# Kernel tuning notes

Measured on AMD Instinct MI355X. Metric: run time of the kernel, lower is better.

Reference implementation:

```python
import jax, jax.numpy as jnp
import numpy as np

B, D, N, C = 2048, 128, 100000, 100
T = 2.0


def setup_inputs() -> dict:
    key = jax.random.key(0)
    k1, k2, k3 = jax.random.split(key, 3)
    x = jax.random.normal(k1, (B, D), dtype=jnp.float32)
    Address = jax.random.normal(k2, (N, D), dtype=jnp.float32)
    M = jax.random.uniform(k3, (N, C), dtype=jnp.float32)
    return {"x": x, "Address": Address, "M": M}


def reference(x, Address, M):
    # dist[b,n] = ||x_b - A_n||_2 via the expanded quadratic form (same as torch mm+norms)
    sq = (-2.0 * (x @ Address.T)
          + jnp.sum(Address * Address, axis=1)[None, :]
          + jnp.sum(x * x, axis=1)[:, None])
    dist = jnp.sqrt(jnp.maximum(sq, 0.0))  # clamp guards fp roundoff negatives
    # softmin over addresses == softmax(-dist/T)
    soft_w = jax.nn.softmax(-dist / T, axis=1)  # (B, N)
    logits = soft_w @ M  # (B, n_classes)
    return logits
```

## Files before the change

### kernel.cpp

```cpp
#include <hip/hip_runtime.h>

#define NTOT 100000
#define BD 128
#define NC 100
#define CP 112
#define BROWS 2048
#define LOG2E 1.4426950408889634f

typedef short short8 __attribute__((ext_vector_type(8)));
typedef float f32x4 __attribute__((ext_vector_type(4)));

__device__ __forceinline__ unsigned short f2bf(float f) {
    union { float f; unsigned u; } v; v.f = f;
    unsigned r = v.u + 0x7FFFu + ((v.u >> 16) & 1u);
    return (unsigned short)(r >> 16);
}

__device__ __forceinline__ unsigned pkbf(float a, float b) {
    unsigned r;
    asm("v_cvt_pk_bf16_f32 %0, %1, %2" : "=v"(r) : "v"(a), "v"(b));
    return r;
}

__device__ __forceinline__ float rawsqrt(float x) {
    float r;
    asm("v_sqrt_f32 %0, %1" : "=v"(r) : "v"(x));
    return r;
}

__device__ __forceinline__ float rawexp2(float x) {
    float r;
    asm("v_exp_f32 %0, %1" : "=v"(r) : "v"(x));
    return r;
}

__device__ __forceinline__ void gload16(const void* g, void* l) {
    __builtin_amdgcn_global_load_lds((const __attribute__((address_space(1))) void*)g,
                                     (__attribute__((address_space(3))) void*)l, 16, 0, 0);
}

__global__ __launch_bounds__(256) void prep_A(const float* __restrict__ A,
                                              unsigned short* __restrict__ Abf,
                                              float* __restrict__ anorm) {
    const int tid = threadIdx.x;
    const int row = blockIdx.x * 16 + (tid >> 4);
    const int g = tid & 15;
    const float* src = A + (size_t)row * BD + g * 8;
    float4 v0 = *(const float4*)src, v1 = *(const float4*)(src + 4);
    uint4 u;
    u.x = pkbf(v0.x, v0.y); u.y = pkbf(v0.z, v0.w);
    u.z = pkbf(v1.x, v1.y); u.w = pkbf(v1.z, v1.w);
    float ss = v0.x*v0.x + v0.y*v0.y + v0.z*v0.z + v0.w*v0.w
             + v1.x*v1.x + v1.y*v1.y + v1.z*v1.z + v1.w*v1.w;
    ss += __shfl_xor(ss, 1); ss += __shfl_xor(ss, 2);
    ss += __shfl_xor(ss, 4); ss += __shfl_xor(ss, 8);
    *(uint4*)((char*)Abf + (size_t)row * 256 + ((g * 16) ^ ((row & 15) << 4))) = u;
    if (g == 0) anorm[row] = ss;
}

__global__ __launch_bounds__(256) void prep_M(const float* __restrict__ M,
                                              unsigned short* __restrict__ Mt) {
    __shared__ __align__(16) unsigned short lm[100 * 264];
    const int t = threadIdx.x;
    const int n0 = blockIdx.x * 256;
    const int rows = min(256, NTOT - n0);
    const float4* Mf4 = (const float4*)(M + (size_t)n0 * NC);
    #pragma unroll
    for (int k = 0; k < 25; ++k) {
        int f = k * 256 + t;
        if (f < rows * 25) {
            int row = (int)(((unsigned)f * 5243u) >> 17);
            int c4 = f - row * 25;
            float4 v = Mf4[f];
            lm[(c4 * 4 + 0) * 264 + row] = f2bf(v.x);
            lm[(c4 * 4 + 1) * 264 + row] = f2bf(v.y);
            lm[(c4 * 4 + 2) * 264 + row] = f2bf(v.z);
            lm[(c4 * 4 + 3) * 264 + row] = f2bf(v.w);
        }
    }
    __syncthreads();
    uint4* Mt4 = (uint4*)Mt;
    const int nb = rows >> 3;
    #pragma unroll
    for (int k = 0; k < 14; ++k) {
        int f = k * 256 + t;
        int c = f >> 5, nblk = f & 31;
        if (nblk < nb) {
            uint4 v = {0u, 0u, 0u, 0u};
            if (c < NC) v = *(const uint4*)&lm[c * 264 + nblk * 8];
            Mt4[(size_t)c * (NTOT / 8) + (n0 >> 3) + nblk] = v;
        }
    }
}

__global__ __launch_bounds__(256, 2) void fused_main(
    const float* __restrict__ x, const unsigned short* __restrict__ Abf,
    const float* __restrict__ anorm, const unsigned short* __restrict__ Mt,
    float* __restrict__ pO, float* __restrict__ pL,
    int cmask, int cshift, int qq, int rr)
{
    __shared__ __align__(16) unsigned short a_lds[2][4096];
    __shared__ __align__(16) unsigned short m_lds[2][3584];
    __shared__ __align__(16) unsigned short p_lds[8][640];

    const int tid = threadIdx.x, wave = tid >> 6, lane = tid & 63;
    const int l15 = lane & 15, lhi = lane >> 4;
    const int bid = blockIdx.x;
    const int chunk = bid & cmask, rg = bid >> cshift;
    const int ts = chunk * qq + (chunk < rr ? chunk : rr);
    const int tiles = (chunk < rr) ? qq + 1 : qq;
    const int n0c = ts * 32;
    const int qbw = rg * 128 + wave * 32;

    short8 qf[2][4];
    float nx[2];
    #pragma unroll
    for (int t = 0; t < 2; ++t) {
        float s = 0.f;
        #pragma unroll
        for (int kk = 0; kk < 4; ++kk) {
            const float* xp = x + (size_t)(qbw + t * 16 + l15) * BD + kk * 32 + lhi * 8;
            float4 v0 = *(const float4*)xp, v1 = *(const float4*)(xp + 4);
            uint4 uu;
            uu.x = pkbf(v0.x, v0.y); uu.y = pkbf(v0.z, v0.w);
            uu.z = pkbf(v1.x, v1.y); uu.w = pkbf(v1.z, v1.w);
            qf[t][kk] = *(short8*)&uu;
            s += v0.x*v0.x + v0.y*v0.y + v0.z*v0.z + v0.w*v0.w
               + v1.x*v1.x + v1.y*v1.y + v1.z*v1.z + v1.w*v1.w;
        }
        s += __shfl_xor(s, 16); s += __shfl_xor(s, 32);
        nx[t] = s;
    }

    const char* aFix = (const char*)Abf + tid * 16;
    const int r0 = tid >> 2, sg0 = ((tid & 3) - r0 - (r0 >> 2)) & 3;
    const char* mFix0 = (const char*)Mt + (size_t)r0 * (NTOT * 2) + sg0 * 16;
    const int L1 = tid + 256, r1 = L1 >> 2, sg1 = ((L1 & 3) - r1 - (r1 >> 2)) & 3;
    const char* mFix1 = (const char*)Mt + (size_t)r1 * (NTOT * 2) + sg1 * 16;

    auto stage = [&](int buf, int t) {
        const int n0 = n0c + t * 32;
        const char* ab = aFix + (size_t)n0 * 256;
        char* al = (char*)&a_lds[buf][0] + tid * 16;
        gload16(ab, al);
        gload16(ab + 4096, al + 4096);
        gload16(mFix0 + (size_t)n0 * 2, (char*)&m_lds[buf][0] + tid * 16);
        if (tid < 192)
            gload16(mFix1 + (size_t)n0 * 2, (char*)&m_lds[buf][0] + (tid + 256) * 16);
    };

    f32x4 Oacc[2][7];
    const f32x4 zf = {0.f, 0.f, 0.f, 0.f};
    #pragma unroll
    for (int t = 0; t < 2; ++t)
        #pragma unroll
        for (int c0 = 0; c0 < 7; ++c0) Oacc[t][c0] = zf;
    float lsum[2] = {0.f, 0.f};

    stage(0, 0);
    __syncthreads();

    for (int it = 0; it < tiles; ++it) {
        const int buf = it & 1;
        const int n0 = n0c + it * 32;
        if (it + 1 < tiles) stage(buf ^ 1, it + 1);

        float an[8];
        #pragma unroll
        for (int j = 0; j < 8; ++j)
            an[j] = anorm[n0 + (j >> 2) * 16 + lhi * 4 + (j & 3)];

        f32x4 s0[2], s1[2];
        s0[0] = zf; s0[1] = zf; s1[0] = zf; s1[1] = zf;
        const char* ab = (const char*)&a_lds[buf][0];
        #pragma unroll
        for (int kk = 0; kk < 4; ++kk) {
            const int sw = (kk * 64 + lhi * 16) ^ (l15 << 4);
            short8 b0 = *(const short8*)(ab + l15 * 256 + sw);
            short8 b1 = *(const short8*)(ab + (16 + l15) * 256 + sw);
            s0[0] = __builtin_amdgcn_mfma_f32_16x16x32_bf16(b0, qf[0][kk], s0[0], 0, 0, 0);
            s1[0] = __builtin_amdgcn_mfma_f32_16x16x32_bf16(b1, qf[0][kk], s1[0], 0, 0, 0);
            s0[1] = __builtin_amdgcn_mfma_f32_16x16x32_bf16(b0, qf[1][kk], s0[1], 0, 0, 0);
            s1[1] = __builtin_amdgcn_mfma_f32_16x16x32_bf16(b1, qf[1][kk], s1[1], 0, 0, 0);
        }

        #pragma unroll
        for (int t = 0; t < 2; ++t) {
            float p[8];
            #pragma unroll
            for (int j = 0; j < 8; ++j) {
                float sv = (j < 4) ? s0[t][j & 3] : s1[t][j & 3];
                float sq = fmaf(sv, -2.f, an[j]) + nx[t];
                float d = rawsqrt(fmaxf(sq, 0.f));
                float pv = rawexp2(d * (-0.5f * LOG2E));
                p[j] = pv;
                lsum[t] += pv;
            }
            char* pw = (char*)&p_lds[wave * 2 + t][0] + l15 * 80 + lhi * 8;
            uint2 w0 = { pkbf(p[0], p[1]), pkbf(p[2], p[3]) };
            uint2 w1 = { pkbf(p[4], p[5]), pkbf(p[6], p[7]) };
            *(uint2*)(pw) = w0;
            *(uint2*)(pw + 32) = w1;
        }

        const short8 pa0 = *(const short8*)((const char*)&p_lds[wave * 2 + 0][0] + l15 * 80 + lhi * 16);
        const short8 pa1 = *(const short8*)((const char*)&p_lds[wave * 2 + 1][0] + l15 * 80 + lhi * 16);
        const char* mb = (const char*)&m_lds[buf][0];
        #pragma unroll
        for (int c0 = 0; c0 < 7; ++c0) {
            const int c = c0 * 16 + l15;
            short8 bm = *(const short8*)(mb + c * 64 + (((lhi + c + (c >> 2)) & 3) * 16));
            Oacc[0][c0] = __builtin_amdgcn_mfma_f32_16x16x32_bf16(pa0, bm, Oacc[0][c0], 0, 0, 0);
            Oacc[1][c0] = __builtin_amdgcn_mfma_f32_16x16x32_bf16(pa1, bm, Oacc[1][c0], 0, 0, 0);
        }

        __syncthreads();
    }

    const size_t crow = (size_t)chunk * BROWS;
    #pragma unroll
    for (int t = 0; t < 2; ++t) {
        float ls = lsum[t];
        ls += __shfl_xor(ls, 16); ls += __shfl_xor(ls, 32);
        #pragma unroll
        for (int c0 = 0; c0 < 7; ++c0)
            #pragma unroll
            for (int r2 = 0; r2 < 4; ++r2)
                pO[(crow + qbw + t * 16 + lhi * 4 + r2) * CP + c0 * 16 + l15] = Oacc[t][c0][r2];
        if (lane < 16) pL[crow + qbw + t * 16 + lane] = ls;
    }
}

__global__ __launch_bounds__(128) void combine(
    const float* __restrict__ pO, const float* __restrict__ pL,
    float* __restrict__ out, int nch)
{
    const int r = blockIdx.x, c = threadIdx.x;
    if (c >= NC) return;
    float acc = 0.f, l = 0.f;
    for (int i = 0; i < nch; ++i) {
        acc += pO[((size_t)i * BROWS + r) * CP + c];
        l   += pL[(size_t)i * BROWS + r];
    }
    out[(size_t)r * NC + c] = acc / l;
}

#define FBNS 16
#define FBCH 6250
#define KV 32
#define AST 136
#define MST 40
#define PST 40

__global__ __launch_bounds__(256, 2) void fused_fb(
    const float* __restrict__ x, const float* __restrict__ A,
    const float* __restrict__ M, float* __restrict__ pO,
    float* __restrict__ pM, float* __restrict__ pL)
{
    __shared__ __align__(16) unsigned short a_lds[KV * AST];
    __shared__ __align__(16) unsigned short mt_lds[CP * MST];
    __shared__ __align__(16) unsigned short p_lds[4][16 * PST];
    __shared__ float anorm_s[KV];

    const int tid  = threadIdx.x;
    const int wave = tid >> 6, lane = tid & 63;
    const int l15  = lane & 15, lhi = lane >> 4;
    const int bid  = blockIdx.x;
    const int chunk = bid & (FBNS - 1);
    const int rg    = bid >> 4;
    const int n0c   = chunk * FBCH;
    const int n1c   = n0c + FBCH;
    const int qbase = rg * 64 + wave * 16;
    const int q     = qbase + l15;

    short8 qf[4];
    float sumsq = 0.f;
    #pragma unroll
    for (int kk = 0; kk < 4; ++kk) {
        const float* xp = x + (size_t)q * BD + kk * 32 + lhi * 8;
        float4 v0 = *(const float4*)xp;
        float4 v1 = *(const float4*)(xp + 4);
        short8 f;
        f[0] = (short)f2bf(v0.x); f[1] = (short)f2bf(v0.y);
        f[2] = (short)f2bf(v0.z); f[3] = (short)f2bf(v0.w);
        f[4] = (short)f2bf(v1.x); f[5] = (short)f2bf(v1.y);
        f[6] = (short)f2bf(v1.z); f[7] = (short)f2bf(v1.w);
        qf[kk] = f;
        sumsq += v0.x*v0.x + v0.y*v0.y + v0.z*v0.z + v0.w*v0.w
               + v1.x*v1.x + v1.y*v1.y + v1.z*v1.z + v1.w*v1.w;
    }
    sumsq += __shfl_xor(sumsq, 16);
    sumsq += __shfl_xor(sumsq, 32);
    float nxr[4];
    #pragma unroll
    for (int r2 = 0; r2 < 4; ++r2) nxr[r2] = __shfl(sumsq, lhi * 4 + r2);

    const f32x4 zf = {0.f, 0.f, 0.f, 0.f};
    f32x4 Oacc[7];
    #pragma unroll
    for (int c = 0; c < 7; ++c) Oacc[c] = zf;
    float mrow[4] = {-1e30f, -1e30f, -1e30f, -1e30f};
    float lrow[4] = {0.f, 0.f, 0.f, 0.f};

    for (int n0 = n0c; n0 < n1c; n0 += KV) {
        __syncthreads();
        {
            int arow = tid >> 3, seg = tid & 7;
            int n = n0 + arow;
            float s2 = 0.f;
            unsigned short* dst = &a_lds[arow * AST + seg * 16];
            if (n < n1c) {
                const float* src = A + (size_t)n * BD + seg * 16;
                #pragma unroll
                for (int j = 0; j < 4; ++j) {
                    float4 v = ((const float4*)src)[j];
                    dst[j*4+0] = f2bf(v.x); dst[j*4+1] = f2bf(v.y);
                    dst[j*4+2] = f2bf(v.z); dst[j*4+3] = f2bf(v.w);
                    s2 += v.x*v.x + v.y*v.y + v.z*v.z + v.w*v.w;
                }
            } else {
                #pragma unroll
                for (int j = 0; j < 16; ++j) dst[j] = 0;
            }
            s2 += __shfl_xor(s2, 1);
            s2 += __shfl_xor(s2, 2);
            s2 += __shfl_xor(s2, 4);
            if (seg == 0) anorm_s[arow] = (n < n1c) ? s2 : 1e18f;
        }
        #pragma unroll
        for (int it = 0; it < 14; ++it) {
            int idx = tid + it * 256;
            int r2 = idx / CP;
            int c  = idx - r2 * CP;
            int n  = n0 + r2;
            float v = (c < NC && n < n1c) ? M[(size_t)n * NC + c] : 0.f;
            mt_lds[c * MST + r2] = f2bf(v);
        }
        __syncthreads();

        f32x4 s[2]; s[0] = zf; s[1] = zf;
        #pragma unroll
        for (int t = 0; t < 2; ++t) {
            #pragma unroll
            for (int kk = 0; kk < 4; ++kk) {
                short8 bf = *(const short8*)&a_lds[(t*16 + l15) * AST + kk*32 + lhi*8];
                s[t] = __builtin_amdgcn_mfma_f32_16x16x32_bf16(qf[kk], bf, s[t], 0, 0, 0);
            }
        }
        float na0 = anorm_s[l15], na1 = anorm_s[16 + l15];

        float pv0[4], pv1[4], fr[4];
        #pragma unroll
        for (int r2 = 0; r2 < 4; ++r2) {
            float s0 = nxr[r2] + na0 - 2.f * s[0][r2];
            float s1 = nxr[r2] + na1 - 2.f * s[1][r2];
            s0 = -0.5f * sqrtf(fmaxf(s0, 0.f));
            s1 = -0.5f * sqrtf(fmaxf(s1, 0.f));
            float v = fmaxf(s0, s1);
            v = fmaxf(v, __shfl_xor(v, 1));
            v = fmaxf(v, __shfl_xor(v, 2));
            v = fmaxf(v, __shfl_xor(v, 4));
            v = fmaxf(v, __shfl_xor(v, 8));
            float mnew = fmaxf(mrow[r2], v);
            float f = exp2f((mrow[r2] - mnew) * LOG2E);
            mrow[r2] = mnew;
            float p0 = exp2f((s0 - mnew) * LOG2E);
            float p1 = exp2f((s1 - mnew) * LOG2E);
            pv0[r2] = p0; pv1[r2] = p1;
            float ps = p0 + p1;
            ps += __shfl_xor(ps, 1);
            ps += __shfl_xor(ps, 2);
            ps += __shfl_xor(ps, 4);
            ps += __shfl_xor(ps, 8);
            lrow[r2] = lrow[r2] * f + ps;
            fr[r2] = f;
        }
        #pragma unroll
        for (int c = 0; c < 7; ++c)
            #pragma unroll
            for (int r2 = 0; r2 < 4; ++r2) Oacc[c][r2] *= fr[r2];

        #pragma unroll
        for (int r2 = 0; r2 < 4; ++r2) {
            p_lds[wave][(lhi*4 + r2) * PST +  0 + l15] = f2bf(pv0[r2]);
            p_lds[wave][(lhi*4 + r2) * PST + 16 + l15] = f2bf(pv1[r2]);
        }
        short8 pa = *(const short8*)&p_lds[wave][l15 * PST + lhi * 8];
        #pragma unroll
        for (int c = 0; c < 7; ++c) {
            short8 bm = *(const short8*)&mt_lds[(c*16 + l15) * MST + lhi * 8];
            Oacc[c] = __builtin_amdgcn_mfma_f32_16x16x32_bf16(pa, bm, Oacc[c], 0, 0, 0);
        }
    }

    const size_t crow = (size_t)chunk * 2048;
    #pragma unroll
    for (int c = 0; c < 7; ++c) {
        #pragma unroll
        for (int r2 = 0; r2 < 4; ++r2) {
            int row = qbase + lhi * 4 + r2;
            pO[(crow + row) * CP + c * 16 + l15] = Oacc[c][r2];
        }
    }
    if (l15 == 0) {
        #pragma unroll
        for (int r2 = 0; r2 < 4; ++r2) {
            int row = qbase + lhi * 4 + r2;
            pM[crow + row] = mrow[r2];
            pL[crow + row] = lrow[r2];
        }
    }
}

__global__ __launch_bounds__(128) void combine_fb(
    const float* __restrict__ pO, const float* __restrict__ pM,
    const float* __restrict__ pL, float* __restrict__ out)
{
    int r = blockIdx.x;
    int c = threadIdx.x;
    float mi[FBNS];
    float mg = -1e30f;
    #pragma unroll
    for (int i = 0; i < FBNS; ++i) { mi[i] = pM[i * 2048 + r]; mg = fmaxf(mg, mi[i]); }
    float w[FBNS];
    float lg = 0.f;
    #pragma unroll
    for (int i = 0; i < FBNS; ++i) {
        w[i] = exp2f((mi[i] - mg) * LOG2E);
        lg += pL[i * 2048 + r] * w[i];
    }
    if (c < NC) {
        float acc = 0.f;
        #pragma unroll
        for (int i = 0; i < FBNS; ++i)
            acc += pO[((size_t)i * 2048 + r) * CP + c] * w[i];
        out[(size_t)r * NC + c] = acc / lg;
    }
}

extern "C" void kernel_launch(void* const* d_in, const int* in_sizes, int n_in,
                              void* d_out, int out_size, void* d_ws, size_t ws_size,
                              hipStream_t stream) {
    const float* x = (const float*)d_in[0];
    const float* A = (const float*)d_in[1];
    const float* M = (const float*)d_in[2];
    float* out = (float*)d_out;

    const size_t BASE = 25600000 + 400000 + 22400000;
    const size_t NEED64 = BASE + (size_t)64 * BROWS * CP * 4 + (size_t)64 * BROWS * 4;
    const size_t NEED32 = BASE + (size_t)32 * BROWS * CP * 4 + (size_t)32 * BROWS * 4;

    if (ws_size >= NEED32) {
        unsigned short* Abf = (unsigned short*)d_ws;
        float* anorm = (float*)(Abf + (size_t)NTOT * BD);
        unsigned short* Mt = (unsigned short*)(anorm + NTOT);
        float* pO = (float*)(Mt + (size_t)CP * NTOT);
        const int nch = (ws_size >= NEED64) ? 64 : 32;
        float* pL = pO + (size_t)nch * BROWS * CP;
        prep_A<<<6250, 256, 0, stream>>>(A, Abf, anorm);
        prep_M<<<391, 256, 0, stream>>>(M, Mt);
        if (nch == 64) {
            fused_main<<<1024, 256, 0, stream>>>(x, Abf, anorm, Mt, pO, pL, 63, 6, 48, 53);
        } else {
            fused_main<<<512, 256, 0, stream>>>(x, Abf, anorm, Mt, pO, pL, 31, 5, 97, 21);
        }
        combine<<<2048, 128, 0, stream>>>(pO, pL, out, nch);
    } else {
        float* pO = (float*)d_ws;
        float* pM = pO + (size_t)FBNS * 2048 * CP;
        float* pL = pM + (size_t)FBNS * 2048;
        fused_fb<<<512, 256, 0, stream>>>(x, A, M, pO, pM, pL);
        combine_fb<<<2048, 128, 0, stream>>>(pO, pM, pL, out);
    }
}
```

Before: 287.9 us.

## Load A and M tiles straight to registers and reduce outputs with atomics

Drops the double-buffered LDS staging of the A and M tiles; each wave now loads its MFMA operands directly from global memory into registers. The per-chunk partial-output buffers and the separate combine kernel are replaced by atomicAdd into the zeroed output and a row-sum array, followed by a small normalize kernel. The intent is to save LDS traffic and the large partial-buffer write and read. In exchange, the four waves of a block each fetch the same A tile, global-load latency is no longer hidden by prefetch, there are many more atomics, and M rows past the 100th are read beyond the now-unpadded Mt buffer.

```diff
diff --git a/kernel.cpp b/kernel.cpp
--- a/kernel.cpp
+++ b/kernel.cpp
@@ -3,7 +3,6 @@
 #define NTOT 100000
 #define BD 128
 #define NC 100
-#define CP 112
 #define BROWS 2048
 #define LOG2E 1.4426950408889634f
 
@@ -32,11 +31,6 @@
     float r;
     asm("v_exp_f32 %0, %1" : "=v"(r) : "v"(x));
     return r;
-}
-
-__device__ __forceinline__ void gload16(const void* g, void* l) {
-    __builtin_amdgcn_global_load_lds((const __attribute__((address_space(1))) void*)g,
-                                     (__attribute__((address_space(3))) void*)l, 16, 0, 0);
 }
 
 __global__ __launch_bounds__(256) void prep_A(const float* __restrict__ A,
@@ -54,7 +48,7 @@
              + v1.x*v1.x + v1.y*v1.y + v1.z*v1.z + v1.w*v1.w;
     ss += __shfl_xor(ss, 1); ss += __shfl_xor(ss, 2);
     ss += __shfl_xor(ss, 4); ss += __shfl_xor(ss, 8);
-    *(uint4*)((char*)Abf + (size_t)row * 256 + ((g * 16) ^ ((row & 15) << 4))) = u;
+    *(uint4*)((char*)Abf + (size_t)row * 256 + g * 16) = u;
     if (g == 0) anorm[row] = ss;
 }
 
@@ -82,25 +76,27 @@
     uint4* Mt4 = (uint4*)Mt;
     const int nb = rows >> 3;
     #pragma unroll
-    for (int k = 0; k < 14; ++k) {
+    for (int k = 0; k < 13; ++k) {
         int f = k * 256 + t;
         int c = f >> 5, nblk = f & 31;
-        if (nblk < nb) {
-            uint4 v = {0u, 0u, 0u, 0u};
-            if (c < NC) v = *(const uint4*)&lm[c * 264 + nblk * 8];
-            Mt4[(size_t)c * (NTOT / 8) + (n0 >> 3) + nblk] = v;
-        }
-    }
-}
-
-__global__ __launch_bounds__(256, 2) void fused_main(
+        if (c < NC && nblk < nb)
+            Mt4[(size_t)c * (NTOT / 8) + (n0 >> 3) + nblk] = *(const uint4*)&lm[c * 264 + nblk * 8];
+    }
+}
+
+__global__ __launch_bounds__(256) void zero_k(float* __restrict__ out,
+                                              float* __restrict__ latom) {
+    int i = blockIdx.x * 256 + threadIdx.x;
+    if (i < BROWS * NC) out[i] = 0.f;
+    if (i < BROWS) latom[i] = 0.f;
+}
+
+__global__ __launch_bounds__(256) void fused_direct(
     const float* __restrict__ x, const unsigned short* __restrict__ Abf,
     const float* __restrict__ anorm, const unsigned short* __restrict__ Mt,
-    float* __restrict__ pO, float* __restrict__ pL,
+    float* __restrict__ out, float* __restrict__ latom,
     int cmask, int cshift, int qq, int rr)
 {
-    __shared__ __align__(16) unsigned short a_lds[2][4096];
-    __shared__ __align__(16) unsigned short m_lds[2][3584];
     __shared__ __align__(16) unsigned short p_lds[8][640];
 
     const int tid = threadIdx.x, wave = tid >> 6, lane = tid & 63;
@@ -132,22 +128,8 @@
         nx[t] = s;
     }
 
-    const char* aFix = (const char*)Abf + tid * 16;
-    const int r0 = tid >> 2, sg0 = ((tid & 3) - r0 - (r0 >> 2)) & 3;
-    const char* mFix0 = (const char*)Mt + (size_t)r0 * (NTOT * 2) + sg0 * 16;
-    const int L1 = tid + 256, r1 = L1 >> 2, sg1 = ((L1 & 3) - r1 - (r1 >> 2)) & 3;
-    const char* mFix1 = (const char*)Mt + (size_t)r1 * (NTOT * 2) + sg1 * 16;
-
-    auto stage = [&](int buf, int t) {
-        const int n0 = n0c + t * 32;
-        const char* ab = aFix + (size_t)n0 * 256;
-        char* al = (char*)&a_lds[buf][0] + tid * 16;
-        gload16(ab, al);
-        gload16(ab + 4096, al + 4096);
-        gload16(mFix0 + (size_t)n0 * 2, (char*)&m_lds[buf][0] + tid * 16);
-        if (tid < 192)
-            gload16(mFix1 + (size_t)n0 * 2, (char*)&m_lds[buf][0] + (tid + 256) * 16);
-    };
+    const char* paB = (const char*)Abf + (size_t)l15 * 256 + lhi * 16;
+    const char* pmB = (const char*)Mt + (size_t)l15 * (NTOT * 2) + lhi * 16;
 
     f32x4 Oacc[2][7];
     const f32x4 zf = {0.f, 0.f, 0.f, 0.f};
@@ -157,31 +139,32 @@
         for (int c0 = 0; c0 < 7; ++c0) Oacc[t][c0] = zf;
     float lsum[2] = {0.f, 0.f};
 
-    stage(0, 0);
-    __syncthreads();
-
     for (int it = 0; it < tiles; ++it) {
-        const int buf = it & 1;
         const int n0 = n0c + it * 32;
-        if (it + 1 < tiles) stage(buf ^ 1, it + 1);
-
-        float an[8];
-        #pragma unroll
-        for (int j = 0; j < 8; ++j)
-            an[j] = anorm[n0 + (j >> 2) * 16 + lhi * 4 + (j & 3)];
+
+        const char* pa = paB + (size_t)n0 * 256;
+        short8 a0[4], a1[4];
+        #pragma unroll
+        for (int kk = 0; kk < 4; ++kk) {
+            a0[kk] = *(const short8*)(pa + kk * 64);
+            a1[kk] = *(const short8*)(pa + 4096 + kk * 64);
+        }
+        const char* pm = pmB + (size_t)n0 * 2;
+        short8 mfr[7];
+        #pragma unroll
+        for (int c0 = 0; c0 < 7; ++c0)
+            mfr[c0] = *(const short8*)(pm + (size_t)c0 * (16 * NTOT * 2));
+        f32x4 an0 = *(const f32x4*)(anorm + n0 + lhi * 4);
+        f32x4 an1 = *(const f32x4*)(anorm + n0 + 16 + lhi * 4);
 
         f32x4 s0[2], s1[2];
         s0[0] = zf; s0[1] = zf; s1[0] = zf; s1[1] = zf;
-        const char* ab = (const char*)&a_lds[buf][0];
         #pragma unroll
         for (int kk = 0; kk < 4; ++kk) {
-            const int sw = (kk * 64 + lhi * 16) ^ (l15 << 4);
-            short8 b0 = *(const short8*)(ab + l15 * 256 + sw);
-            short8 b1 = *(const short8*)(ab + (16 + l15) * 256 + sw);
-            s0[0] = __builtin_amdgcn_mfma_f32_16x16x32_bf16(b0, qf[0][kk], s0[0], 0, 0, 0);
-            s1[0] = __builtin_amdgcn_mfma_f32_16x16x32_bf16(b1, qf[0][kk], s1[0], 0, 0, 0);
-            s0[1] = __builtin_amdgcn_mfma_f32_16x16x32_bf16(b0, qf[1][kk], s0[1], 0, 0, 0);
-            s1[1] = __builtin_amdgcn_mfma_f32_16x16x32_bf16(b1, qf[1][kk], s1[1], 0, 0, 0);
+            s0[0] = __builtin_amdgcn_mfma_f32_16x16x32_bf16(a0[kk], qf[0][kk], s0[0], 0, 0, 0);
+            s1[0] = __builtin_amdgcn_mfma_f32_16x16x32_bf16(a1[kk], qf[0][kk], s1[0], 0, 0, 0);
+            s0[1] = __builtin_amdgcn_mfma_f32_16x16x32_bf16(a0[kk], qf[1][kk], s0[1], 0, 0, 0);
+            s1[1] = __builtin_amdgcn_mfma_f32_16x16x32_bf16(a1[kk], qf[1][kk], s1[1], 0, 0, 0);
         }
 
         #pragma unroll
@@ -190,7 +173,8 @@
             #pragma unroll
             for (int j = 0; j < 8; ++j) {
                 float sv = (j < 4) ? s0[t][j & 3] : s1[t][j & 3];
-                float sq = fmaf(sv, -2.f, an[j]) + nx[t];
+                float av = (j < 4) ? an0[j & 3] : an1[j & 3];
+                float sq = fmaf(sv, -2.f, av) + nx[t];
                 float d = rawsqrt(fmaxf(sq, 0.f));
                 float pv = rawexp2(d * (-0.5f * LOG2E));
                 p[j] = pv;
@@ -205,44 +189,39 @@
 
         const short8 pa0 = *(const short8*)((const char*)&p_lds[wave * 2 + 0][0] + l15 * 80 + lhi * 16);
         const short8 pa1 = *(const short8*)((const char*)&p_lds[wave * 2 + 1][0] + l15 * 80 + lhi * 16);
-        const char* mb = (const char*)&m_lds[buf][0];
         #pragma unroll
         for (int c0 = 0; c0 < 7; ++c0) {
-            const int c = c0 * 16 + l15;
-            short8 bm = *(const short8*)(mb + c * 64 + (((lhi + c + (c >> 2)) & 3) * 16));
-            Oacc[0][c0] = __builtin_amdgcn_mfma_f32_16x16x32_bf16(pa0, bm, Oacc[0][c0], 0, 0, 0);
-            Oacc[1][c0] = __builtin_amdgcn_mfma_f32_16x16x32_bf16(pa1, bm, Oacc[1][c0], 0, 0, 0);
-        }
-
-        __syncthreads();
-    }
-
-    const size_t crow = (size_t)chunk * BROWS;
+            Oacc[0][c0] = __builtin_amdgcn_mfma_f32_16x16x32_bf16(pa0, mfr[c0], Oacc[0][c0], 0, 0, 0);
+            Oacc[1][c0] = __builtin_amdgcn_mfma_f32_16x16x32_bf16(pa1, mfr[c0], Oacc[1][c0], 0, 0, 0);
+        }
+
+        __builtin_amdgcn_s_barrier();
+    }
+
     #pragma unroll
     for (int t = 0; t < 2; ++t) {
         float ls = lsum[t];
         ls += __shfl_xor(ls, 16); ls += __shfl_xor(ls, 32);
-        #pragma unroll
-        for (int c0 = 0; c0 < 7; ++c0)
-            #pragma unroll
-            for (int r2 = 0; r2 < 4; ++r2)
-                pO[(crow + qbw + t * 16 + lhi * 4 + r2) * CP + c0 * 16 + l15] = Oacc[t][c0][r2];
-        if (lane < 16) pL[crow + qbw + t * 16 + lane] = ls;
-    }
-}
-
-__global__ __launch_bounds__(128) void combine(
-    const float* __restrict__ pO, const float* __restrict__ pL,
-    float* __restrict__ out, int nch)
-{
+        const int c =  0 * 0 + l15;
+        #pragma unroll
+        for (int c0 = 0; c0 < 7; ++c0) {
+            const int cc = c0 * 16 + c;
+            if (cc < NC) {
+                #pragma unroll
+                for (int r2 = 0; r2 < 4; ++r2) {
+                    const int row = qbw + t * 16 + lhi * 4 + r2;
+                    atomicAdd(&out[(size_t)row * NC + cc], Oacc[t][c0][r2]);
+                }
+            }
+        }
+        if (lane < 16) atomicAdd(&latom[qbw + t * 16 + lane], ls);
+    }
+}
+
+__global__ __launch_bounds__(128) void normalize(float* __restrict__ out,
+                                                 const float* __restrict__ latom) {
     const int r = blockIdx.x, c = threadIdx.x;
-    if (c >= NC) return;
-    float acc = 0.f, l = 0.f;
-    for (int i = 0; i < nch; ++i) {
-        acc += pO[((size_t)i * BROWS + r) * CP + c];
-        l   += pL[(size_t)i * BROWS + r];
-    }
-    out[(size_t)r * NC + c] = acc / l;
+    if (c < NC) out[(size_t)r * NC + c] /= latom[r];
 }
 
 #define FBNS 16
@@ -251,6 +230,7 @@
 #define AST 136
 #define MST 40
 #define PST 40
+#define CP 112
 
 __global__ __launch_bounds__(256, 2) void fused_fb(
     const float* __restrict__ x, const float* __restrict__ A,
@@ -446,25 +426,17 @@
     const float* M = (const float*)d_in[2];
     float* out = (float*)d_out;
 
-    const size_t BASE = 25600000 + 400000 + 22400000;
-    const size_t NEED64 = BASE + (size_t)64 * BROWS * CP * 4 + (size_t)64 * BROWS * 4;
-    const size_t NEED32 = BASE + (size_t)32 * BROWS * CP * 4 + (size_t)32 * BROWS * 4;
-
-    if (ws_size >= NEED32) {
+    const size_t NEED = 25600000 + 400000 + 20000000 + 8192;
+    if (ws_size >= NEED) {
         unsigned short* Abf = (unsigned short*)d_ws;
         float* anorm = (float*)(Abf + (size_t)NTOT * BD);
         unsigned short* Mt = (unsigned short*)(anorm + NTOT);
-        float* pO = (float*)(Mt + (size_t)CP * NTOT);
-        const int nch = (ws_size >= NEED64) ? 64 : 32;
-        float* pL = pO + (size_t)nch * BROWS * CP;
+        float* latom = (float*)(Mt + (size_t)NC * NTOT);
         prep_A<<<6250, 256, 0, stream>>>(A, Abf, anorm);
         prep_M<<<391, 256, 0, stream>>>(M, Mt);
-        if (nch == 64) {
-            fused_main<<<1024, 256, 0, stream>>>(x, Abf, anorm, Mt, pO, pL, 63, 6, 48, 53);
-        } else {
-            fused_main<<<512, 256, 0, stream>>>(x, Abf, anorm, Mt, pO, pL, 31, 5, 97, 21);
-        }
-        combine<<<2048, 128, 0, stream>>>(pO, pL, out, nch);
+        zero_k<<<800, 256, 0, stream>>>(out, latom);
+        fused_direct<<<1024, 256, 0, stream>>>(x, Abf, anorm, Mt, out, latom, 63, 6, 48, 53);
+        normalize<<<2048, 128, 0, stream>>>(out, latom);
     } else {
         float* pO = (float*)d_ws;
         float* pM = pO + (size_t)FBNS * 2048 * CP;
```

Result: slower. 465.8 us (+61.8%).
